# Kernel optimization log

Hardware: AMD Instinct MI355X
Metric: run time of the kernel (lower is better)

Reference implementation:

```python
import jax, jax.numpy as jnp
import numpy as np

B, N, C = 2, 2048, 1152
H = 16
HD = C // H  # 72
SCALE = HD ** -0.5
NEG = -100000000.0  # -1e8 bias for fp32 masked positions


def setup_inputs() -> dict:
    key = jax.random.key(0)
    k1, k2, k3, k4, k5 = jax.random.split(key, 5)
    x = jax.random.normal(k1, (B, N, C), dtype=jnp.float32)
    attn_mask = jax.random.randint(k2, (B, N), 0, 2, dtype=jnp.int32)
    w_qkv = jax.random.normal(k3, (3 * C, C), dtype=jnp.float32) * 0.02
    w_proj = jax.random.normal(k4, (C, C), dtype=jnp.float32) * 0.02
    b_proj = jax.random.normal(k5, (C,), dtype=jnp.float32) * 0.02
    return {"x": x, "attn_mask": attn_mask, "w_qkv": w_qkv, "w_proj": w_proj, "b_proj": b_proj}


def reference(x, attn_mask, w_qkv, w_proj, b_proj):
    # qkv projection: [B,N,3C] -> [3,B,H,N,HD]
    qkv = (x @ w_qkv.T).reshape(B, N, 3, H, HD).transpose(2, 0, 3, 1, 4)
    q, k, v = qkv[0], qkv[1], qkv[2]

    # additive mask bias from outer product of per-token 0/1 mask
    m = attn_mask.astype(x.dtype)          # [B,N]
    mm = m[:, :, None] * m[:, None, :]      # [B,N,N]
    bias = jnp.where(mm == 0, NEG, jnp.where(mm == 1, 0.0, mm))
    bias = bias[:, None, :, :]              # [B,1,N,N] broadcast over heads

    # math-branch attention: full QK^T, bias add, softmax, NaN patch, AV
    attn = jnp.einsum('bhqd,bhkd->bhqk', q, k) * SCALE + bias
    attn = jax.nn.softmax(attn, axis=-1)
    attn = jnp.where(jnp.isnan(attn), 0.0, attn)
    out = jnp.einsum('bhqk,bhkd->bqhd', attn, v).reshape(B, N, C)

    return out @ w_proj.T + b_proj
```

## Files before the change

### kernel.cpp

```cpp
#include <hip/hip_runtime.h>

#define B_   2
#define N_   2048
#define C_   1152
#define H_   16
#define HD_  72
#define QKV_W 3456
#define SCALE_ 0.11785113019775793f
#define NEG_  -100000000.0f
#define HDP  96
#define HDV  80
#define PRE_  0.1700219068852255f
#define FMAX_ 4.0f
#define KNEG_ 16384.0f

typedef _Float16  f16x8  __attribute__((ext_vector_type(8)));
typedef _Float16  f16x4  __attribute__((ext_vector_type(4)));
typedef float     f32x4  __attribute__((ext_vector_type(4)));

#define GLOAD_LDS16(gp, lp)                                                    \
  __builtin_amdgcn_global_load_lds(                                            \
      (const __attribute__((address_space(1))) void*)(gp),                     \
      (__attribute__((address_space(3))) void*)(lp), 16, 0, 0)

static __device__ __forceinline__ unsigned pack2h(_Float16 a, _Float16 b) {
  union { _Float16 h[2]; unsigned u; } u;
  u.h[0] = a; u.h[1] = b; return u.u;
}

__global__ __launch_bounds__(256)
void split3_f16(const float* __restrict__ x, const float* __restrict__ wq,
                const float* __restrict__ wp,
                _Float16* __restrict__ xf, _Float16* __restrict__ wqf,
                _Float16* __restrict__ wpf,
                _Float16* __restrict__ Qf, _Float16* __restrict__ Kf,
                _Float16* __restrict__ Vt, const int* __restrict__ mask,
                float* __restrict__ meanAcc, int nmv,
                int n8x, int n8q, int n8p) {
  int i = blockIdx.x * 256 + threadIdx.x;
  if (i < nmv) meanAcc[i] = 0.0f;

  const float* src = nullptr; _Float16* dst = nullptr;
  if (i < n8x) { src = x; dst = xf; }
  else {
    i -= n8x;
    if (i < n8q) { src = wq; dst = wqf; }
    else {
      i -= n8q;
      if (i < n8p) { src = wp; dst = wpf; }
      else {
        i -= n8p;
        if (i < 32 * 2048 * 3) {
          const int bh = i / (2048 * 3);
          int rem = i - bh * (2048 * 3);
          const int n = rem / 3, c3 = rem - (rem / 3) * 3;
          f16x8 qp = {}, kp = {};
          if (c3 == 0) {
            qp[0] = (_Float16)1.0f;
            const int kb = (mask[(bh >> 4) * N_ + n] != 0);
            kp[0] = (_Float16)(kb ? -FMAX_ : -KNEG_);
          }
          const size_t base = ((size_t)bh * N_ + n) * HDP + 72 + c3 * 8;
          *(f16x8*)(Qf + base) = qp;
          *(f16x8*)(Kf + base) = kp;
          return;
        }
        i -= 32 * 2048 * 3;
        if (i < 32 * 8 * 256) {
          const int bh = i >> 11, rem = i & 2047;
          const int dp = rem >> 8, nc = rem & 255;
          f16x8 z = {};
          *(f16x8*)(Vt + ((size_t)bh * HDV + 72 + dp) * N_ + nc * 8) = z;
        }
        return;
      }
    }
  }

  const float4* p = (const float4*)src + (size_t)i * 2;
  float4 a = p[0], b = p[1];
  float xs[8] = {a.x, a.y, a.z, a.w, b.x, b.y, b.z, b.w};
  f16x8 hv;
#pragma unroll
  for (int r = 0; r < 8; ++r) hv[r] = (_Float16)xs[r];
  *(f16x8*)(dst + (size_t)i * 8) = hv;
}

__global__ __launch_bounds__(256)
void gemm_f16(const _Float16* __restrict__ A, const _Float16* __restrict__ Bm,
              const float* __restrict__ bias, float* __restrict__ Cout,
              int M, int Nn, int K) {
  __shared__ uint4 lds[2][1024];

  const int tid  = threadIdx.x;
  const int wv   = tid >> 6;
  const int lane = tid & 63;
  const int wm   = wv >> 1;
  const int wn   = wv & 1;
  const int m0 = blockIdx.x * 128, n0 = blockIdx.y * 128;

  const char* gp[4];
  int gd[4];
#pragma unroll
  for (int i = 0; i < 4; ++i) {
    const int gid = wv * 4 + i;
    if (gid < 8) {
      gd[i] = gid * 64;
      gp[i] = (const char*)(A + (size_t)(m0 + gid * 16 + (lane & 15)) * K +
                            ((lane >> 4) << 3));
    } else {
      const int g2 = gid - 8;
      gd[i] = 512 + g2 * 64;
      gp[i] = (const char*)(Bm + (size_t)(n0 + g2 * 16 + (lane & 15)) * K +
                            ((lane >> 4) << 3));
    }
  }

#pragma unroll
  for (int i = 0; i < 4; ++i) {
    GLOAD_LDS16(gp[i], &lds[0][gd[i]]);
    gp[i] += 64;
  }

  f32x4 acc[4][4] = {};
  const int nk = K >> 5;

  for (int kt = 0; kt < nk; ++kt) {
    const int cur = kt & 1, nxt = cur ^ 1;
    __syncthreads();

    if (kt < nk - 1) {
#pragma unroll
      for (int i = 0; i < 4; ++i) {
        GLOAD_LDS16(gp[i], &lds[nxt][gd[i]]);
        gp[i] += 64;
      }
    }

    const uint4* cbuf = lds[cur];
    f16x8 af[4], bf[4];
#pragma unroll
    for (int t = 0; t < 4; ++t) {
      af[t] = *(const f16x8*)&cbuf[(wm * 4 + t) * 64 + lane];
      bf[t] = *(const f16x8*)&cbuf[512 + (wn * 4 + t) * 64 + lane];
    }
#pragma unroll
    for (int i = 0; i < 4; ++i)
#pragma unroll
      for (int j = 0; j < 4; ++j)
        acc[i][j] = __builtin_amdgcn_mfma_f32_16x16x32_f16(af[i], bf[j], acc[i][j], 0, 0, 0);
  }

  const int cl = lane & 15, rq = (lane >> 4) << 2;
#pragma unroll
  for (int j = 0; j < 4; ++j) {
    const int col = n0 + (wn * 4 + j) * 16 + cl;
    const float bv = bias ? bias[col] : 0.0f;
#pragma unroll
    for (int i = 0; i < 4; ++i) {
      const int row = m0 + (wm * 4 + i) * 16 + rq;
#pragma unroll
      for (int r = 0; r < 4; ++r)
        Cout[(size_t)(row + r) * Nn + col] = acc[i][j][r] + bv;
    }
  }
}

__global__ __launch_bounds__(256)
void gemm_qkv_fused(const _Float16* __restrict__ A, const _Float16* __restrict__ Bm,
                    _Float16* __restrict__ Qf, _Float16* __restrict__ Kf,
                    _Float16* __restrict__ Vt, float* __restrict__ meanAcc) {
  __shared__ uint4 lds[2][1024];

  const int K = C_;
  const int tid  = threadIdx.x;
  const int wv   = tid >> 6;
  const int lane = tid & 63;
  const int wm   = wv >> 1;
  const int wn   = wv & 1;
  const int m0 = blockIdx.x * 128, n0 = blockIdx.y * 128;

  const char* gp[4];
  int gd[4];
#pragma unroll
  for (int i = 0; i < 4; ++i) {
    const int gid = wv * 4 + i;
    if (gid < 8) {
      gd[i] = gid * 64;
      gp[i] = (const char*)(A + (size_t)(m0 + gid * 16 + (lane & 15)) * K +
                            ((lane >> 4) << 3));
    } else {
      const int g2 = gid - 8;
      gd[i] = 512 + g2 * 64;
      gp[i] = (const char*)(Bm + (size_t)(n0 + g2 * 16 + (lane & 15)) * K +
                            ((lane >> 4) << 3));
    }
  }

#pragma unroll
  for (int i = 0; i < 4; ++i) {
    GLOAD_LDS16(gp[i], &lds[0][gd[i]]);
    gp[i] += 64;
  }

  f32x4 acc[4][4] = {};
  const int nk = K >> 5;

  for (int kt = 0; kt < nk; ++kt) {
    const int cur = kt & 1, nxt = cur ^ 1;
    __syncthreads();

    if (kt < nk - 1) {
#pragma unroll
      for (int i = 0; i < 4; ++i) {
        GLOAD_LDS16(gp[i], &lds[nxt][gd[i]]);
        gp[i] += 64;
      }
    }

    const uint4* cbuf = lds[cur];
    f16x8 af[4], bf[4];
#pragma unroll
    for (int t = 0; t < 4; ++t) {
      af[t] = *(const f16x8*)&cbuf[(wm * 4 + t) * 64 + lane];
      bf[t] = *(const f16x8*)&cbuf[512 + (wn * 4 + t) * 64 + lane];
    }
#pragma unroll
    for (int i = 0; i < 4; ++i)
#pragma unroll
      for (int j = 0; j < 4; ++j)
        acc[i][j] = __builtin_amdgcn_mfma_f32_16x16x32_f16(af[i], bf[j], acc[i][j], 0, 0, 0);
  }

  const int s = n0 / C_;
  const int b = m0 >> 11;
  const int nloc = m0 & 2047;
  const int cl = lane & 15, rq = (lane >> 4) << 2;

  if (s < 2) {
    _Float16* dst = (s == 0) ? Qf : Kf;
    const float sc = (s == 0) ? PRE_ : 1.0f;
#pragma unroll
    for (int j = 0; j < 4; ++j) {
      const int col  = n0 + (wn * 4 + j) * 16 + cl;
      const int dseg = col - s * C_;
      const int h = dseg / HD_, hd = dseg - h * HD_;
      _Float16* base =
          dst + ((size_t)(b * H_ + h) * N_ + nloc + wm * 64) * HDP + hd;
#pragma unroll
      for (int i = 0; i < 4; ++i) {
        const int r0 = i * 16 + rq;
#pragma unroll
        for (int r = 0; r < 4; ++r)
          base[(size_t)(r0 + r) * HDP] = (_Float16)(acc[i][j][r] * sc);
      }
    }
  } else {
#pragma unroll
    for (int j = 0; j < 4; ++j) {
      const int col = n0 + (wn * 4 + j) * 16 + cl;
      const int dv  = col - 2 * C_;
      const int h = dv / HD_, hd = dv - h * HD_;
      const int bh = b * H_ + h;
      _Float16* base = Vt + ((size_t)bh * HDV + hd) * N_ + nloc + wm * 64;
      float colsum = 0.0f;
#pragma unroll
      for (int i = 0; i < 4; ++i) {
        const int r0 = i * 16 + rq;
        *(uint2*)(base + r0) =
            make_uint2(pack2h((_Float16)acc[i][j][0], (_Float16)acc[i][j][1]),
                       pack2h((_Float16)acc[i][j][2], (_Float16)acc[i][j][3]));
        colsum += (acc[i][j][0] + acc[i][j][1]) + (acc[i][j][2] + acc[i][j][3]);
      }
      colsum += __shfl_xor(colsum, 16);
      colsum += __shfl_xor(colsum, 32);
      if ((lane >> 4) == 0)
        atomicAdd(&meanAcc[bh * HD_ + hd], colsum);
    }
  }
}

__global__ __launch_bounds__(256)
void attn_mfma(const _Float16* __restrict__ Qf, const _Float16* __restrict__ Kf,
               const _Float16* __restrict__ Vt, const float* __restrict__ meanV,
               const int* __restrict__ mask, _Float16* __restrict__ att) {
  const int bh = blockIdx.x, qt = blockIdx.y;
  const int b = bh >> 4, h = bh & 15;
  const int tid = threadIdx.x, wv = tid >> 6, lane = tid & 63;
  const int lq = lane & 15;
  const int lg = lane >> 4;
  const int q0 = qt * 128;

  __shared__ uint4 lds[2][22 * 64];
  __shared__ __align__(16) _Float16 Pbuf[2][4][16][72];

  f16x8 qh[2][3];
#pragma unroll
  for (int bd = 0; bd < 2; ++bd) {
    const size_t qoff =
        ((size_t)bh * N_ + q0 + bd * 64 + wv * 16 + lq) * HDP + lg * 8;
#pragma unroll
    for (int c = 0; c < 3; ++c)
      qh[bd][c] = *(const f16x8*)(Qf + qoff + c * 32);
  }

  const _Float16* kb = Kf + (size_t)bh * N_ * HDP;
  const _Float16* vb = Vt + (size_t)bh * HDV * (size_t)N_;

  const int gstart = (wv < 2) ? wv * 6 : 12 + (wv - 2) * 5;
  const int gcount = (wv < 2) ? 6 : 5;
  const char* gptr[6];
  long gstepB[6];
  int gdst[6];
#pragma unroll
  for (int i = 0; i < 6; ++i) {
    int gid = gstart + i;
    if (gid > 21) gid = 21;
    gdst[i] = gid * 64;
    if (gid < 12) {
      const int tile = gid / 3, ch = gid - tile * 3;
      gptr[i] = (const char*)(kb + (size_t)(tile * 16 + lq) * HDP + ch * 32 + lg * 8);
      gstepB[i] = 64 * HDP * 2;
    } else {
      const int v = gid - 12, td = v >> 1, ck = v & 1;
      gptr[i] = (const char*)(vb + (size_t)(td * 16 + lq) * N_ + ck * 32 + lg * 8);
      gstepB[i] = 64 * 2;
    }
  }

#pragma unroll
  for (int i = 0; i < 6; ++i)
    if (i < gcount) {
      GLOAD_LDS16(gptr[i], &lds[0][gdst[i]]);
      gptr[i] += gstepB[i];
    }

  float l_run[2] = {0.0f, 0.0f};
  f32x4 Oacc[2][5] = {};

  for (int kt = 0; kt < N_ / 64; ++kt) {
    const int cur = kt & 1, nxt = cur ^ 1;
    __syncthreads();

    if (kt < N_ / 64 - 1) {
#pragma unroll
      for (int i = 0; i < 6; ++i)
        if (i < gcount) {
          GLOAD_LDS16(gptr[i], &lds[nxt][gdst[i]]);
          gptr[i] += gstepB[i];
        }
    }

    const uint4* cbuf = lds[cur];

    f32x4 s[2][4] = {};
#pragma unroll
    for (int ch = 0; ch < 3; ++ch)
#pragma unroll
      for (int t = 0; t < 4; ++t) {
        f16x8 kf = *(const f16x8*)&cbuf[(t * 3 + ch) * 64 + lane];
        s[0][t] = __builtin_amdgcn_mfma_f32_16x16x32_f16(kf, qh[0][ch], s[0][t], 0, 0, 0);
        s[1][t] = __builtin_amdgcn_mfma_f32_16x16x32_f16(kf, qh[1][ch], s[1][t], 0, 0, 0);
      }

#pragma unroll
    for (int bd = 0; bd < 2; ++bd) {
      float psum = 0.0f;
#pragma unroll
      for (int t = 0; t < 4; ++t) {
        const float p0 = exp2f(s[bd][t][0]);
        const float p1 = exp2f(s[bd][t][1]);
        const float p2 = exp2f(s[bd][t][2]);
        const float p3 = exp2f(s[bd][t][3]);
        psum += (p0 + p1) + (p2 + p3);
        *(uint2*)&Pbuf[bd][wv][lq][t * 16 + 4 * lg] =
            make_uint2(pack2h((_Float16)p0, (_Float16)p1),
                       pack2h((_Float16)p2, (_Float16)p3));
      }
      l_run[bd] += psum;
    }

#pragma unroll
    for (int ck = 0; ck < 2; ++ck) {
      f16x8 pf0 = *(const f16x8*)&Pbuf[0][wv][lq][ck * 32 + lg * 8];
      f16x8 pf1 = *(const f16x8*)&Pbuf[1][wv][lq][ck * 32 + lg * 8];
#pragma unroll
      for (int td = 0; td < 5; ++td) {
        f16x8 vf = *(const f16x8*)&cbuf[(12 + td * 2 + ck) * 64 + lane];
        Oacc[0][td] = __builtin_amdgcn_mfma_f32_16x16x32_f16(vf, pf0, Oacc[0][td], 0, 0, 0);
        Oacc[1][td] = __builtin_amdgcn_mfma_f32_16x16x32_f16(vf, pf1, Oacc[1][td], 0, 0, 0);
      }
    }
  }

  __syncthreads();
  float* osc = (float*)lds;
  float* myo = osc + wv * 16 * 81;
  const int rq = lane >> 2, jj = lane & 3;

#pragma unroll
  for (int bd = 0; bd < 2; ++bd) {
    float l = l_run[bd];
    l += __shfl_xor(l, 16);
    l += __shfl_xor(l, 32);
    const float inv = 1.0f / l;
#pragma unroll
    for (int td = 0; td < 5; ++td)
#pragma unroll
      for (int r = 0; r < 4; ++r)
        myo[lq * 81 + td * 16 + 4 * lg + r] = Oacc[bd][td][r] * inv;
    __syncthreads();

    const int q = q0 + bd * 64 + wv * 16 + rq;
    const int qm = (mask[b * N_ + q] != 0);
    const float* rowp = myo + rq * 81 + jj * 18;
    const float* mvp  = meanV + bh * HD_ + jj * 18;
    const size_t obase = ((size_t)(b * N_) + q) * C_ + h * HD_ + jj * 18;
#pragma unroll
    for (int e = 0; e < 9; ++e) {
      const float a = qm ? rowp[2 * e]     : mvp[2 * e]     * (1.0f / 2048.0f);
      const float c = qm ? rowp[2 * e + 1] : mvp[2 * e + 1] * (1.0f / 2048.0f);
      *(unsigned*)(att + obase + 2 * e) = pack2h((_Float16)a, (_Float16)c);
    }
    __syncthreads();
  }
}

__global__ __launch_bounds__(256)
void gemm64_nt(const float* __restrict__ A, const float* __restrict__ Bm,
               const float* __restrict__ bias, float* __restrict__ C,
               int M, int N, int K) {
  __shared__ __align__(16) float As[32][68];
  __shared__ __align__(16) float Bs[32][68];
  const int tid = threadIdx.x;
  const int tx = tid & 15, ty = tid >> 4;
  const int m0 = blockIdx.x * 64, n0 = blockIdx.y * 64;
  float acc[4][4] = {};
  for (int k0 = 0; k0 < K; k0 += 32) {
#pragma unroll
    for (int i = 0; i < 2; ++i) {
      const int idx = tid + i * 256;
      const int row = idx >> 3, kc = (idx & 7) << 2;
      float4 a = *(const float4*)(A + (size_t)(m0 + row) * K + k0 + kc);
      As[kc + 0][row] = a.x; As[kc + 1][row] = a.y;
      As[kc + 2][row] = a.z; As[kc + 3][row] = a.w;
      float4 b = *(const float4*)(Bm + (size_t)(n0 + row) * K + k0 + kc);
      Bs[kc + 0][row] = b.x; Bs[kc + 1][row] = b.y;
      Bs[kc + 2][row] = b.z; Bs[kc + 3][row] = b.w;
    }
    __syncthreads();
#pragma unroll
    for (int k = 0; k < 32; ++k) {
      float4 av4 = *(const float4*)&As[k][ty << 2];
      float4 bv4 = *(const float4*)&Bs[k][tx << 2];
      float av[4] = {av4.x, av4.y, av4.z, av4.w};
      float bv[4] = {bv4.x, bv4.y, bv4.z, bv4.w};
#pragma unroll
      for (int i = 0; i < 4; ++i)
#pragma unroll
        for (int j = 0; j < 4; ++j) acc[i][j] += av[i] * bv[j];
    }
    __syncthreads();
  }
#pragma unroll
  for (int i = 0; i < 4; ++i) {
    const int row = m0 + (ty << 2) + i, col = n0 + (tx << 2);
    float4 v = make_float4(acc[i][0], acc[i][1], acc[i][2], acc[i][3]);
    if (bias) {
      v.x += bias[col + 0]; v.y += bias[col + 1];
      v.z += bias[col + 2]; v.w += bias[col + 3];
    }
    *(float4*)(C + (size_t)row * N + col) = v;
  }
}

__global__ __launch_bounds__(256)
void attn_kernel(const float* __restrict__ qkv, const int* __restrict__ mask,
                 float* __restrict__ out) {
  const int qt = blockIdx.x, h = blockIdx.y, b = blockIdx.z;
  const int tid = threadIdx.x;
  const int q0 = qt * 64;
  __shared__ __align__(16) float qT[HD_][68];
  __shared__ __align__(16) float kT[HD_][68];
  __shared__ __align__(16) float vT[HD_][68];
  __shared__ float rowm[64], rowl[64], rowa[64];
  __shared__ float biask[64];
  __shared__ int   mq[64];
  float (*ps)[68] = (float (*)[68])kT;
  const float* qg = qkv + (size_t)(b * N_ + q0) * QKV_W + h * HD_;
  for (int idx = tid; idx < 64 * HD_; idx += 256) {
    const int qi = idx / HD_, d = idx % HD_;
    qT[d][qi] = qg[(size_t)qi * QKV_W + d];
  }
  if (tid < 64) {
    rowm[tid] = -1e30f; rowl[tid] = 0.0f;
    mq[tid] = mask[b * N_ + q0 + tid];
  }
  const int sqg = tid >> 4, skg = tid & 15;
  const int oqg = tid >> 3, ods = tid & 7;
  float o[4][9];
#pragma unroll
  for (int i = 0; i < 4; ++i)
#pragma unroll
    for (int dd = 0; dd < 9; ++dd) o[i][dd] = 0.0f;
  __syncthreads();
  for (int kt = 0; kt < N_ / 64; ++kt) {
    const int k0 = kt * 64;
    const float* kg = qkv + (size_t)(b * N_ + k0) * QKV_W + C_ + h * HD_;
    const float* vg = qkv + (size_t)(b * N_ + k0) * QKV_W + 2 * C_ + h * HD_;
    for (int idx = tid; idx < 64 * HD_; idx += 256) {
      const int kj = idx / HD_, d = idx % HD_;
      kT[d][kj] = kg[(size_t)kj * QKV_W + d];
      vT[d][kj] = vg[(size_t)kj * QKV_W + d];
    }
    if (tid < 64) biask[tid] = (mask[b * N_ + k0 + tid] != 0) ? 0.0f : NEG_;
    __syncthreads();
    float sacc[4][4] = {};
    for (int d = 0; d < HD_; ++d) {
      float4 qv4 = *(const float4*)&qT[d][sqg << 2];
      float4 kv4 = *(const float4*)&kT[d][skg << 2];
      float qa[4] = {qv4.x, qv4.y, qv4.z, qv4.w};
      float ka[4] = {kv4.x, kv4.y, kv4.z, kv4.w};
#pragma unroll
      for (int i = 0; i < 4; ++i)
#pragma unroll
        for (int j = 0; j < 4; ++j) sacc[i][j] += qa[i] * ka[j];
    }
    __syncthreads();
#pragma unroll
    for (int i = 0; i < 4; ++i) {
      const int qi = (sqg << 2) + i;
      const int qm2 = mq[qi];
#pragma unroll
      for (int j = 0; j < 4; ++j) {
        const int kj = (skg << 2) + j;
        const float bias = (qm2 != 0) ? biask[kj] : NEG_;
        ps[qi][kj] = sacc[i][j] * SCALE_ + bias;
      }
    }
    __syncthreads();
    if (tid < 64) {
      float mt = -1e30f;
#pragma unroll
      for (int j4 = 0; j4 < 16; ++j4) {
        float4 p4 = *(const float4*)&ps[tid][j4 << 2];
        mt = fmaxf(mt, fmaxf(fmaxf(p4.x, p4.y), fmaxf(p4.z, p4.w)));
      }
      const float mo = rowm[tid];
      const float nm = fmaxf(mo, mt);
      const float a = __expf(mo - nm);
      float sum = 0.0f;
#pragma unroll
      for (int j4 = 0; j4 < 16; ++j4) {
        float4 p4 = *(const float4*)&ps[tid][j4 << 2];
        p4.x = __expf(p4.x - nm); p4.y = __expf(p4.y - nm);
        p4.z = __expf(p4.z - nm); p4.w = __expf(p4.w - nm);
        sum += p4.x + p4.y + p4.z + p4.w;
        *(float4*)&ps[tid][j4 << 2] = p4;
      }
      rowl[tid] = rowl[tid] * a + sum;
      rowm[tid] = nm;
      rowa[tid] = a;
    }
    __syncthreads();
    if (tid < 128) {
#pragma unroll
      for (int i = 0; i < 4; ++i) {
        const float a = rowa[(oqg << 2) + i];
#pragma unroll
        for (int dd = 0; dd < 9; ++dd) o[i][dd] *= a;
      }
      for (int k4 = 0; k4 < 16; ++k4) {
        float4 pv4[4];
#pragma unroll
        for (int i = 0; i < 4; ++i)
          pv4[i] = *(const float4*)&ps[(oqg << 2) + i][k4 << 2];
        float pa[4][4];
#pragma unroll
        for (int i = 0; i < 4; ++i) {
          pa[i][0] = pv4[i].x; pa[i][1] = pv4[i].y;
          pa[i][2] = pv4[i].z; pa[i][3] = pv4[i].w;
        }
#pragma unroll
        for (int dd = 0; dd < 9; ++dd) {
          float4 vv4 = *(const float4*)&vT[ods * 9 + dd][k4 << 2];
          float va[4] = {vv4.x, vv4.y, vv4.z, vv4.w};
#pragma unroll
          for (int i = 0; i < 4; ++i)
            o[i][dd] += pa[i][0] * va[0] + pa[i][1] * va[1] +
                        pa[i][2] * va[2] + pa[i][3] * va[3];
        }
      }
    }
    __syncthreads();
  }
  if (tid < 128) {
#pragma unroll
    for (int i = 0; i < 4; ++i) {
      const int qi = (oqg << 2) + i;
      const float inv = 1.0f / rowl[qi];
      const size_t base = (size_t)(b * N_ + q0 + qi) * C_ + h * HD_ + ods * 9;
#pragma unroll
      for (int dd = 0; dd < 9; ++dd) out[base + dd] = o[i][dd] * inv;
    }
  }
}

extern "C" void kernel_launch(void* const* d_in, const int* in_sizes, int n_in,
                              void* d_out, int out_size, void* d_ws, size_t ws_size,
                              hipStream_t stream) {
  (void)in_sizes; (void)n_in; (void)out_size;

  const float* x      = (const float*)d_in[0];
  const int*   mask   = (const int*)  d_in[1];
  const float* w_qkv  = (const float*)d_in[2];
  const float* w_proj = (const float*)d_in[3];
  const float* b_proj = (const float*)d_in[4];
  float* out = (float*)d_out;

  const size_t XE = (size_t)B_ * N_ * C_;
  const size_t WQ = (size_t)QKV_W * C_;
  const size_t WP = (size_t)C_ * C_;
  const size_t QKVE = (size_t)B_ * N_ * QKV_W;
  const size_t QKE  = (size_t)B_ * H_ * N_ * HDP;
  const size_t VTE  = (size_t)B_ * H_ * HDV * N_;
  const int    MVN  = B_ * H_ * HD_;

  char* w = (char*)d_ws;
  _Float16* att  = (_Float16*)w;
  _Float16* x_f  = att + XE;
  _Float16* wq_f = x_f + XE;
  _Float16* wp_f = wq_f + WQ;
  _Float16* Qf   = wp_f + WP;
  _Float16* Kf   = Qf + QKE;
  _Float16* Vt   = Kf + QKE;
  float* meanAcc = (float*)(Vt + VTE);
  const size_t need = (size_t)((char*)(meanAcc + MVN) - w);

  if (ws_size >= need) {
    const int n8x = (int)(XE / 8), n8q = (int)(WQ / 8), n8p = (int)(WP / 8);
    const int npadQK = 32 * 2048 * 3;
    const int npadV  = 32 * 8 * 256;
    const int total  = n8x + n8q + n8p + npadQK + npadV;
    split3_f16<<<(total + 255) / 256, 256, 0, stream>>>(
        x, w_qkv, w_proj, x_f, wq_f, wp_f, Qf, Kf, Vt, mask,
        meanAcc, MVN, n8x, n8q, n8p);

    gemm_qkv_fused<<<dim3(32, 27), 256, 0, stream>>>(x_f, wq_f, Qf, Kf, Vt,
                                                     meanAcc);

    attn_mfma<<<dim3(32, 16), 256, 0, stream>>>(Qf, Kf, Vt, meanAcc, mask, att);

    gemm_f16<<<dim3(32, 9), 256, 0, stream>>>(att, wp_f, b_proj, out,
                                              B_ * N_, C_, C_);
  } else {
    float* qkv_f = (float*)d_ws;
    float* att_f = qkv_f + QKVE;
    gemm64_nt<<<dim3(64, 54), 256, 0, stream>>>(x, w_qkv, nullptr, qkv_f,
                                                B_ * N_, QKV_W, C_);
    attn_kernel<<<dim3(32, 16, 2), 256, 0, stream>>>(qkv_f, mask, att_f);
    gemm64_nt<<<dim3(64, 18), 256, 0, stream>>>(att_f, w_proj, b_proj, out,
                                                B_ * N_, C_, C_);
  }
}
```

Before: 281.3 us.

## Fold softmax row-sum into PV MFMA via ones column; use pkrtz converts and swizzle tiles

Padding row 72 of the transposed V is filled with ones, so the PV MFMA also accumulates the softmax denominator. This removes the per-tile scalar psum accumulation and the final shuffle reduction. Float-to-half packing now uses the hardware cvt_pkrtz instruction in several places. The two GEMM kernels also remap blockIdx.x so the order in which M tiles are visited changes, aiming for better cache locality. Because pkrtz rounds toward zero, results differ slightly, and the denominator is now summed from fp16-rounded probabilities.

Result: no change. 276.0 us (-1.9%).

```diff
diff --git a/kernel.cpp b/kernel.cpp
--- a/kernel.cpp
+++ b/kernel.cpp
@@ -26,6 +26,12 @@
 static __device__ __forceinline__ unsigned pack2h(_Float16 a, _Float16 b) {
   union { _Float16 h[2]; unsigned u; } u;
   u.h[0] = a; u.h[1] = b; return u.u;
+}
+typedef __fp16 fp16v2_builtin __attribute__((ext_vector_type(2)));
+static __device__ __forceinline__ unsigned pkrtz(float a, float b) {
+  union { fp16v2_builtin h; unsigned u; } u;
+  u.h = __builtin_amdgcn_cvt_pkrtz(a, b);
+  return u.u;
 }
 
 __global__ __launch_bounds__(256)
@@ -70,6 +76,9 @@
           const int bh = i >> 11, rem = i & 2047;
           const int dp = rem >> 8, nc = rem & 255;
           f16x8 z = {};
+          if (dp == 0)
+#pragma unroll
+            for (int r = 0; r < 8; ++r) z[r] = (_Float16)1.0f;
           *(f16x8*)(Vt + ((size_t)bh * HDV + 72 + dp) * N_ + nc * 8) = z;
         }
         return;
@@ -97,7 +106,9 @@
   const int lane = tid & 63;
   const int wm   = wv >> 1;
   const int wn   = wv & 1;
-  const int m0 = blockIdx.x * 128, n0 = blockIdx.y * 128;
+  const int bx   = blockIdx.x;
+  const int mt   = (bx & 7) * 4 + (bx >> 3);
+  const int m0 = mt * 128, n0 = blockIdx.y * 128;
 
   const char* gp[4];
   int gd[4];
@@ -178,7 +189,9 @@
   const int lane = tid & 63;
   const int wm   = wv >> 1;
   const int wn   = wv & 1;
-  const int m0 = blockIdx.x * 128, n0 = blockIdx.y * 128;
+  const int bx   = blockIdx.x;
+  const int mt   = (bx & 7) * 4 + (bx >> 3);
+  const int m0 = mt * 128, n0 = blockIdx.y * 128;
 
   const char* gp[4];
   int gd[4];
@@ -268,8 +281,8 @@
       for (int i = 0; i < 4; ++i) {
         const int r0 = i * 16 + rq;
         *(uint2*)(base + r0) =
-            make_uint2(pack2h((_Float16)acc[i][j][0], (_Float16)acc[i][j][1]),
-                       pack2h((_Float16)acc[i][j][2], (_Float16)acc[i][j][3]));
+            make_uint2(pkrtz(acc[i][j][0], acc[i][j][1]),
+                       pkrtz(acc[i][j][2], acc[i][j][3]));
         colsum += (acc[i][j][0] + acc[i][j][1]) + (acc[i][j][2] + acc[i][j][3]);
       }
       colsum += __shfl_xor(colsum, 16);
@@ -335,7 +348,6 @@
       gptr[i] += gstepB[i];
     }
 
-  float l_run[2] = {0.0f, 0.0f};
   f32x4 Oacc[2][5] = {};
 
   for (int kt = 0; kt < N_ / 64; ++kt) {
@@ -364,21 +376,16 @@
       }
 
 #pragma unroll
-    for (int bd = 0; bd < 2; ++bd) {
-      float psum = 0.0f;
+    for (int bd = 0; bd < 2; ++bd)
 #pragma unroll
       for (int t = 0; t < 4; ++t) {
         const float p0 = exp2f(s[bd][t][0]);
         const float p1 = exp2f(s[bd][t][1]);
         const float p2 = exp2f(s[bd][t][2]);
         const float p3 = exp2f(s[bd][t][3]);
-        psum += (p0 + p1) + (p2 + p3);
         *(uint2*)&Pbuf[bd][wv][lq][t * 16 + 4 * lg] =
-            make_uint2(pack2h((_Float16)p0, (_Float16)p1),
-                       pack2h((_Float16)p2, (_Float16)p3));
-      }
-      l_run[bd] += psum;
-    }
+            make_uint2(pkrtz(p0, p1), pkrtz(p2, p3));
+      }
 
 #pragma unroll
     for (int ck = 0; ck < 2; ++ck) {
@@ -400,9 +407,7 @@
 
 #pragma unroll
   for (int bd = 0; bd < 2; ++bd) {
-    float l = l_run[bd];
-    l += __shfl_xor(l, 16);
-    l += __shfl_xor(l, 32);
+    const float l = __shfl(Oacc[bd][4][0], 32 + lq);
     const float inv = 1.0f / l;
 #pragma unroll
     for (int td = 0; td < 5; ++td)
@@ -420,7 +425,7 @@
     for (int e = 0; e < 9; ++e) {
       const float a = qm ? rowp[2 * e]     : mvp[2 * e]     * (1.0f / 2048.0f);
       const float c = qm ? rowp[2 * e + 1] : mvp[2 * e + 1] * (1.0f / 2048.0f);
-      *(unsigned*)(att + obase + 2 * e) = pack2h((_Float16)a, (_Float16)c);
+      *(unsigned*)(att + obase + 2 * e) = pkrtz(a, c);
     }
     __syncthreads();
   }
```
